# Optimization experiments

Hardware: AMD Instinct MI355X
Metric: run time of the kernel (lower is better)

## Reference

```python
import jax, jax.numpy as jnp
import numpy as np

B, N, C, H = 8, 1025, 512, 8
G = 32  # grid size; S = G*G = N-1


def setup_inputs() -> dict:
    key = jax.random.key(0)
    ks = jax.random.split(key, 5)
    return {
        "x": jax.random.normal(ks[0], (B, N, C), dtype=jnp.float32),
        "qkv_w": jax.random.normal(ks[1], (3 * C, C), dtype=jnp.float32) * (C ** -0.5),
        "proj_w": jax.random.normal(ks[2], (C, C), dtype=jnp.float32) * (C ** -0.5),
        "proj_b": jnp.zeros((C,), dtype=jnp.float32),
        "wg_w": jax.random.normal(ks[3], (H, 64), dtype=jnp.float32) * 0.125,
        "wg_b": jnp.zeros((H,), dtype=jnp.float32),
    }


def _geometry_bias(wg_w, wg_b):
    # BoxRelationalEmbedding on a fixed 32x32 grid; batch-independent, so computed once.
    S = G * G
    xs = jnp.arange(G, dtype=jnp.float32)
    px = jnp.repeat(xs, G)   # px_min: row index per flattened cell
    py = jnp.tile(xs, G)     # py_min: col index per flattened cell
    rx0, ry0 = px / G, py / G
    rx1, ry1 = (px + 1.0) / G, (py + 1.0) / G
    cx = 0.5 * (rx0 + rx1)
    cy = 0.5 * (ry0 + ry1)
    w = rx1 - rx0 + 1.0
    h = ry1 - ry0 + 1.0
    dx = jnp.log(jnp.clip(jnp.abs((cx[:, None] - cx[None, :]) / w[:, None]), 1e-3, None))
    dy = jnp.log(jnp.clip(jnp.abs((cy[:, None] - cy[None, :]) / h[:, None]), 1e-3, None))
    dw = jnp.log(w[:, None] / w[None, :])
    dh = jnp.log(h[:, None] / h[None, :])
    pos = jnp.stack([dx, dy, dw, dh], axis=-1)  # [S,S,4]
    dim_mat = 1.0 / jnp.power(1000.0, jnp.arange(8, dtype=jnp.float32) / 8.0)  # dim_g/8 = 8 freqs
    mul = (100.0 * pos)[..., None] * dim_mat        # [S,S,4,8]
    mul = mul.reshape(S, S, 32)
    emb = jnp.concatenate([jnp.sin(mul), jnp.cos(mul)], axis=-1)  # [S,S,64]
    rgw = jax.nn.relu(jnp.einsum('ijd,hd->hij', emb, wg_w) + wg_b[:, None, None])  # [H,S,S]
    rgw = jnp.log(jnp.clip(rgw, 1e-6, None))
    # pad zero column (dim 3 cat of t1) then zero row (dim 2 cat of t2) -> [H, S+1, S+1]
    return jnp.pad(rgw, ((0, 0), (1, 0), (1, 0)))


def reference(x, qkv_w, proj_w, proj_b, wg_w, wg_b):
    b, n, c = x.shape
    hd = c // H
    scale = hd ** -0.5
    bias = _geometry_bias(wg_w, wg_b)  # [H, n, n]
    qkv = (x @ qkv_w.T).reshape(b, n, 3, H, hd)
    q, k, v = qkv[:, :, 0], qkv[:, :, 1], qkv[:, :, 2]  # each [b,n,H,hd]
    attn = jnp.einsum('bihd,bjhd->bhij', q, k) * scale + bias[None]
    attn = jax.nn.softmax(attn, axis=-1)
    out = jnp.einsum('bhij,bjhd->bihd', attn, v).reshape(b, n, c)
    return out @ proj_w.T + proj_b
```

## Files before the change

kernel.cpp:

```cpp
#include <hip/hip_runtime.h>
#include <hip/hip_bf16.h>
#include <math.h>

#define B_  8
#define N_  1025
#define C_  512
#define H_  8
#define HD_ 64
#define M_  (B_ * N_)
#define VCS 2048
#define VST 36

typedef __attribute__((ext_vector_type(8))) short short8;
typedef __attribute__((ext_vector_type(4))) float f32x4;

__device__ inline unsigned short bf16u(float x) {
    __hip_bfloat16 t = __float2bfloat16(x);
    return *(unsigned short*)&t;
}
__device__ inline void load_lds16(const void* g, void* l) {
    __builtin_amdgcn_global_load_lds(
        (const __attribute__((address_space(1))) unsigned int*)g,
        (__attribute__((address_space(3))) unsigned int*)l, 16, 0, 0);
}

#define PER_ ((size_t)B_ * H_ * N_ * HD_)
#define SZ_QKVW (3 * C_ * C_)
#define SZ_PRJW (C_ * C_)
#define CAST_BLKS ((4198400 + 786432 + 262144) / 4 / 256)

__global__ void prep_kernel(const float* __restrict__ x,
                            const float* __restrict__ qkv_w,
                            const float* __restrict__ proj_w,
                            const float* __restrict__ wg_w,
                            const float* __restrict__ wg_b,
                            unsigned short* __restrict__ xb,
                            unsigned short* __restrict__ wqkvb,
                            unsigned short* __restrict__ wprjb,
                            float* __restrict__ tab) {
    int blk = blockIdx.x;
    int tid = threadIdx.x;
    if (blk < 32) {
        int idx = blk * 256 + tid;
        int h = idx >> 10;
        int a = (idx >> 5) & 31;
        int b = idx & 31;
        float dx = logf(fmaxf((float)a * (1.0f / 33.0f), 0.001f));
        float dy = logf(fmaxf((float)b * (1.0f / 33.0f), 0.001f));
        const float* w = wg_w + h * 64;
        float acc = wg_b[h];
#pragma unroll
        for (int k = 0; k < 8; k++) {
            float f = powf(1000.0f, -(float)k * 0.125f);
            float X = 100.0f * dx * f;
            float Y = 100.0f * dy * f;
            acc += w[k]      * sinf(X);
            acc += w[8 + k]  * sinf(Y);
            acc += w[32 + k] * cosf(X);
            acc += w[40 + k] * cosf(Y);
            acc += w[48 + k] + w[56 + k];
        }
        tab[idx] = logf(fmaxf(fmaxf(acc, 0.0f), 1e-6f));
        return;
    }
    long i4 = ((long)(blk - 32) * 256 + tid) * 4;
    const float* src;
    unsigned short* dst;
    long off;
    if (i4 < (long)PER_)                    { src = x;      dst = xb;    off = i4; }
    else if (i4 < (long)PER_ + SZ_QKVW)     { src = qkv_w;  dst = wqkvb; off = i4 - PER_; }
    else                                    { src = proj_w; dst = wprjb; off = i4 - PER_ - SZ_QKVW; }
    float4 v = *(const float4*)(src + off);
    ushort4 p;
    p.x = bf16u(v.x); p.y = bf16u(v.y); p.z = bf16u(v.z); p.w = bf16u(v.w);
    *(ushort4*)(dst + off) = p;
}

#define GK 512

__global__ __launch_bounds__(256) void gemm_qkv_mfma(
        const unsigned short* __restrict__ A, const unsigned short* __restrict__ W,
        unsigned short* __restrict__ qb, unsigned short* __restrict__ kb,
        unsigned short* __restrict__ vtc) {
    __shared__ __align__(16) unsigned short As[128 * 32];
    __shared__ __align__(16) unsigned short Bs[128 * 32];
    int tid = threadIdx.x;
    int w = tid >> 6, lane = tid & 63;
    int quad = lane >> 4, l16 = lane & 15;
    int m0 = blockIdx.y * 128;
    int n0 = blockIdx.x * 128;
    int wr = (w >> 1) * 64, wc = (w & 1) * 64;

    int c0 = tid, c1 = tid + 256;
    int a_r0 = min(m0 + (c0 >> 2), M_ - 1), a_c0 = (c0 & 3) * 8;
    int a_r1 = min(m0 + (c1 >> 2), M_ - 1), a_c1 = (c1 & 3) * 8;
    int b_r0 = n0 + (c0 >> 2), b_r1 = n0 + (c1 >> 2);

    int which = n0 >> 9;
    int h = ((n0 + wc) >> 6) & 7;

    f32x4 acc[4][4];
    const f32x4 zero4 = {0.f, 0.f, 0.f, 0.f};
#pragma unroll
    for (int mi = 0; mi < 4; mi++)
#pragma unroll
        for (int ni = 0; ni < 4; ni++) acc[mi][ni] = zero4;

    if (which < 2) {
        for (int k0 = 0; k0 < GK; k0 += 32) {
            __syncthreads();
            load_lds16(A + (size_t)a_r0 * GK + k0 + a_c0, &As[w * 512]);
            load_lds16(A + (size_t)a_r1 * GK + k0 + a_c1, &As[2048 + w * 512]);
            load_lds16(W + (size_t)b_r0 * GK + k0 + a_c0, &Bs[w * 512]);
            load_lds16(W + (size_t)b_r1 * GK + k0 + a_c1, &Bs[2048 + w * 512]);
            __syncthreads();
            short8 af[4], bf[4];
#pragma unroll
            for (int mi = 0; mi < 4; mi++)
                af[mi] = *(const short8*)&As[(wr + mi * 16 + l16) * 32 + quad * 8];
#pragma unroll
            for (int ni = 0; ni < 4; ni++)
                bf[ni] = *(const short8*)&Bs[(wc + ni * 16 + l16) * 32 + quad * 8];
#pragma unroll
            for (int mi = 0; mi < 4; mi++)
#pragma unroll
                for (int ni = 0; ni < 4; ni++)
                    acc[mi][ni] = __builtin_amdgcn_mfma_f32_16x16x32_bf16(
                        bf[ni], af[mi], acc[mi][ni], 0, 0, 0);
        }
        unsigned short* dst = (which == 0) ? qb : kb;
        float sc = (which == 0) ? 0.125f : 1.0f;
#pragma unroll
        for (int mi = 0; mi < 4; mi++) {
            int m = m0 + wr + mi * 16 + l16;
            if (m < M_) {
                int bb = m / N_;
                int i  = m - bb * N_;
                unsigned short* row = dst + ((size_t)(bb * H_ + h) * N_ + i) * HD_;
#pragma unroll
                for (int ni = 0; ni < 4; ni++) {
                    ushort4 pk;
                    pk.x = bf16u(acc[mi][ni][0] * sc);
                    pk.y = bf16u(acc[mi][ni][1] * sc);
                    pk.z = bf16u(acc[mi][ni][2] * sc);
                    pk.w = bf16u(acc[mi][ni][3] * sc);
                    *(ushort4*)(row + ni * 16 + quad * 4) = pk;
                }
            }
        }
    } else {
        for (int k0 = 0; k0 < GK; k0 += 32) {
            __syncthreads();
            load_lds16(A + (size_t)a_r0 * GK + k0 + a_c0, &As[w * 512]);
            load_lds16(A + (size_t)a_r1 * GK + k0 + a_c1, &As[2048 + w * 512]);
            load_lds16(W + (size_t)b_r0 * GK + k0 + a_c0, &Bs[w * 512]);
            load_lds16(W + (size_t)b_r1 * GK + k0 + a_c1, &Bs[2048 + w * 512]);
            __syncthreads();
            short8 af[4], bf[4];
#pragma unroll
            for (int mi = 0; mi < 4; mi++)
                af[mi] = *(const short8*)&As[(wr + mi * 16 + l16) * 32 + quad * 8];
#pragma unroll
            for (int ni = 0; ni < 4; ni++)
                bf[ni] = *(const short8*)&Bs[(wc + ni * 16 + l16) * 32 + quad * 8];
#pragma unroll
            for (int mi = 0; mi < 4; mi++)
#pragma unroll
                for (int ni = 0; ni < 4; ni++)
                    acc[mi][ni] = __builtin_amdgcn_mfma_f32_16x16x32_bf16(
                        af[mi], bf[ni], acc[mi][ni], 0, 0, 0);
        }
#pragma unroll
        for (int mi = 0; mi < 4; mi++)
#pragma unroll
            for (int reg = 0; reg < 4; reg++) {
                int m = m0 + wr + mi * 16 + quad * 4 + reg;
                if (m < M_) {
                    int bb = m / N_;
                    int i  = m - bb * N_;
                    int ch = i >> 5, key = i & 31;
                    size_t base = ((size_t)(bb * H_ + h) * VST + ch) * VCS + key;
#pragma unroll
                    for (int ni = 0; ni < 4; ni++)
                        vtc[base + (size_t)(ni * 16 + l16) * 32] = bf16u(acc[mi][ni][reg]);
                }
            }
    }
}

__global__ __launch_bounds__(256) void gemm_proj_mfma(
        const unsigned short* __restrict__ A, const unsigned short* __restrict__ W,
        const float* __restrict__ bias, float* __restrict__ out) {
    __shared__ __align__(16) unsigned short As[128 * 32];
    __shared__ __align__(16) unsigned short Bs[128 * 32];
    int tid = threadIdx.x;
    int w = tid >> 6, lane = tid & 63;
    int quad = lane >> 4, l16 = lane & 15;
    int m0 = blockIdx.y * 128;
    int n0 = blockIdx.x * 128;
    int wr = (w >> 1) * 64, wc = (w & 1) * 64;

    int c0 = tid, c1 = tid + 256;
    int a_r0 = min(m0 + (c0 >> 2), M_ - 1), a_c0 = (c0 & 3) * 8;
    int a_r1 = min(m0 + (c1 >> 2), M_ - 1), a_c1 = (c1 & 3) * 8;
    int b_r0 = n0 + (c0 >> 2), b_r1 = n0 + (c1 >> 2);

    f32x4 acc[4][4];
    const f32x4 zero4 = {0.f, 0.f, 0.f, 0.f};
#pragma unroll
    for (int mi = 0; mi < 4; mi++)
#pragma unroll
        for (int ni = 0; ni < 4; ni++) acc[mi][ni] = zero4;

    for (int k0 = 0; k0 < GK; k0 += 32) {
        __syncthreads();
        load_lds16(A + (size_t)a_r0 * GK + k0 + a_c0, &As[w * 512]);
        load_lds16(A + (size_t)a_r1 * GK + k0 + a_c1, &As[2048 + w * 512]);
        load_lds16(W + (size_t)b_r0 * GK + k0 + a_c0, &Bs[w * 512]);
        load_lds16(W + (size_t)b_r1 * GK + k0 + a_c1, &Bs[2048 + w * 512]);
        __syncthreads();
        short8 af[4], bf[4];
#pragma unroll
        for (int mi = 0; mi < 4; mi++)
            af[mi] = *(const short8*)&As[(wr + mi * 16 + l16) * 32 + quad * 8];
#pragma unroll
        for (int ni = 0; ni < 4; ni++)
            bf[ni] = *(const short8*)&Bs[(wc + ni * 16 + l16) * 32 + quad * 8];
#pragma unroll
        for (int mi = 0; mi < 4; mi++)
#pragma unroll
            for (int ni = 0; ni < 4; ni++)
                acc[mi][ni] = __builtin_amdgcn_mfma_f32_16x16x32_bf16(
                    af[mi], bf[ni], acc[mi][ni], 0, 0, 0);
    }

    float bvals[4];
#pragma unroll
    for (int ni = 0; ni < 4; ni++) bvals[ni] = bias[n0 + wc + ni * 16 + l16];
#pragma unroll
    for (int mi = 0; mi < 4; mi++)
#pragma unroll
        for (int reg = 0; reg < 4; reg++) {
            int m = m0 + wr + mi * 16 + quad * 4 + reg;
            if (m < M_) {
                float* row = out + (size_t)m * C_ + n0 + wc;
#pragma unroll
                for (int ni = 0; ni < 4; ni++)
                    row[ni * 16 + l16] = acc[mi][ni][reg] + bvals[ni];
            }
        }
}

#define RT_ 144

__global__ __launch_bounds__(576) void attn_fused(
        const unsigned short* __restrict__ qg,
        const unsigned short* __restrict__ kg,
        const unsigned short* __restrict__ vtc,
        const float* __restrict__ tab,
        unsigned short* __restrict__ ob) {
    __shared__ __align__(16) unsigned short Ks[2][8192];
    __shared__ __align__(16) unsigned short Vs[2][8192];
    __shared__ __align__(16) unsigned short Pw[9][16 * 40];
    __shared__ float tabs[1089];

    int tid = threadIdx.x;
    int w = tid >> 6, lane = tid & 63;
    int quad = lane >> 4, l16 = lane & 15;

    int lin = blockIdx.x;
    int xcd = lin & 7;
    int u = lin >> 3;
    int bhi = u & 7;
    int mt = u >> 3;
    int bh = xcd * 8 + bhi;
    int b = bh >> 3, h = bh & 7;

    const unsigned short* qp = qg + (size_t)bh * N_ * HD_;
    const unsigned short* kp = kg + (size_t)bh * N_ * HD_;
    const unsigned short* vp = vtc + (size_t)bh * VST * VCS;

    for (int i = tid; i < 1024; i += 576)
        tabs[(i >> 5) * 33 + (i & 31)] = tab[h * 1024 + i];

    short8 qf[2];
    {
        int row = min(mt * RT_ + w * 16 + l16, N_ - 1);
        qf[0] = *(const short8*)(qp + (size_t)row * HD_ + quad * 8);
        qf[1] = *(const short8*)(qp + (size_t)row * HD_ + 32 + quad * 8);
    }

    int rpx[4], rpy[4];
    bool rz[4];
#pragma unroll
    for (int reg = 0; reg < 4; reg++) {
        int r = mt * RT_ + w * 16 + quad * 4 + reg;
        int ri = min(max(r - 1, 0), N_ - 2);
        rpx[reg] = ri >> 5;
        rpy[reg] = ri & 31;
        rz[reg] = (r == 0);
    }

    f32x4 o_acc[4], l_acc;
    const f32x4 zero4 = {0.f, 0.f, 0.f, 0.f};
#pragma unroll
    for (int g2 = 0; g2 < 4; g2++) o_acc[g2] = zero4;
    l_acc = zero4;
    short8 ones;
    {
        short one_bf = (short)0x3F80;
#pragma unroll
        for (int j = 0; j < 8; j++) ones[j] = one_bf;
    }

    auto stage = [&](int t, int buf) {
        if (w < 8) {
#pragma unroll
            for (int r2 = 0; r2 < 2; r2++) {
                int ch = r2 * 512 + tid;
                int ct = ch >> 7, rem = ch & 127;
                int oct = rem >> 4, k16 = rem & 15;
                int key = min(t * 128 + ct * 16 + k16, N_ - 1);
                load_lds16(kp + (size_t)key * HD_ + oct * 8,
                           &Ks[buf][(r2 * 512 + w * 64) * 8]);
                load_lds16(vp + ((size_t)t * 4 * VCS) + (size_t)ch * 8,
                           &Vs[buf][(r2 * 512 + w * 64) * 8]);
            }
        }
    };

    stage(0, 0);

#pragma unroll 1
    for (int t = 0; t < 9; t++) {
        int buf = t & 1;
        __syncthreads();
        if (t < 8) stage(t + 1, buf ^ 1);

        f32x4 s[8];
#pragma unroll
        for (int ct = 0; ct < 8; ct++) {
            short8 b0 = *(const short8*)&Ks[buf][(ct * 128 + quad * 16 + l16) * 8];
            short8 b1 = *(const short8*)&Ks[buf][(ct * 128 + (4 + quad) * 16 + l16) * 8];
            s[ct] = __builtin_amdgcn_mfma_f32_16x16x32_bf16(qf[0], b0, zero4, 0, 0, 0);
            s[ct] = __builtin_amdgcn_mfma_f32_16x16x32_bf16(qf[1], b1, s[ct], 0, 0, 0);
        }

#pragma unroll
        for (int ks = 0; ks < 4; ks++) {
#pragma unroll
            for (int ctl = 0; ctl < 2; ctl++) {
                int ct = ks * 2 + ctl;
                int col = t * 128 + ct * 16 + l16;
                int ji = col - 1;
                int cx = ji >> 5, cy = ji & 31;
                bool cz = (col == 0), co = (col >= N_);
#pragma unroll
                for (int reg = 0; reg < 4; reg++) {
                    float bia = 0.f;
                    if (!rz[reg] && !cz) {
                        int da = __sad(rpx[reg], cx, 0u);
                        int db = __sad(rpy[reg], cy, 0u);
                        bia = tabs[da * 33 + db];
                    }
                    float p = co ? 0.f : __expf(s[ct][reg] + bia);
                    Pw[w][(quad * 4 + reg) * 40 + ctl * 16 + l16] = bf16u(p);
                }
            }
            short8 pf = *(const short8*)&Pw[w][l16 * 40 + quad * 8];
            const unsigned short* vcp = &Vs[buf][ks * 2048 + quad * 8];
#pragma unroll
            for (int g2 = 0; g2 < 4; g2++) {
                short8 vf = *(const short8*)(vcp + (g2 * 16 + l16) * 32);
                o_acc[g2] = __builtin_amdgcn_mfma_f32_16x16x32_bf16(
                    pf, vf, o_acc[g2], 0, 0, 0);
            }
            l_acc = __builtin_amdgcn_mfma_f32_16x16x32_bf16(pf, ones, l_acc, 0, 0, 0);
        }
    }

#pragma unroll
    for (int reg = 0; reg < 4; reg++) {
        int r = mt * RT_ + w * 16 + quad * 4 + reg;
        if (r < N_) {
            float inv = 1.0f / l_acc[reg];
            unsigned short* orow = ob + ((size_t)b * N_ + r) * C_ + h * HD_ + l16;
#pragma unroll
            for (int g2 = 0; g2 < 4; g2++)
                orow[g2 * 16] = bf16u(o_acc[g2][reg] * inv);
        }
    }
}

extern "C" void kernel_launch(void* const* d_in, const int* in_sizes, int n_in,
                              void* d_out, int out_size, void* d_ws, size_t ws_size,
                              hipStream_t stream) {
    const float* x      = (const float*)d_in[0];
    const float* qkv_w  = (const float*)d_in[1];
    const float* proj_w = (const float*)d_in[2];
    const float* proj_b = (const float*)d_in[3];
    const float* wg_w   = (const float*)d_in[4];
    const float* wg_b   = (const float*)d_in[5];
    float* out = (float*)d_out;

    const size_t per = PER_;
    char* ws = (char*)d_ws;
    float* tab            = (float*)ws;
    unsigned short* xb    = (unsigned short*)(ws + (32 << 10));
    unsigned short* wqkvb = xb + per;
    unsigned short* wprjb = wqkvb + (size_t)SZ_QKVW;
    unsigned short* qb    = wprjb + (size_t)SZ_PRJW;
    unsigned short* kb    = qb + per;
    unsigned short* vtc   = kb + per;
    unsigned short* ob    = vtc + (size_t)64 * VST * VCS;

    prep_kernel<<<32 + CAST_BLKS, 256, 0, stream>>>(x, qkv_w, proj_w, wg_w, wg_b,
                                                    xb, wqkvb, wprjb, tab);
    gemm_qkv_mfma<<<dim3(12, 65), 256, 0, stream>>>(xb, wqkvb, qb, kb, vtc);
    attn_fused<<<8 * 8 * 8, 576, 0, stream>>>(qb, kb, vtc, tab, ob);
    gemm_proj_mfma<<<dim3(4, 65), 256, 0, stream>>>(ob, wprjb, proj_b, out);
}
```

Baseline: 210.4 us.

## Swizzle V tile LDS layout and unify QKV GEMM loop with transposed V store

The QKV GEMM now runs a single k-loop with swapped MFMA operands for all three outputs. The V branch writes the transposed chunked layout from the swapped accumulator orientation, so each lane stores consecutive keys instead of strided scalars. In the attention kernel the V tile is loaded into LDS with an XOR swizzle of its 16-byte chunks, and the reads apply the same permutation, to cut LDS bank conflicts when fetching V fragments. The swizzle must match exactly between the global gather and the LDS reads or the output will be wrong.

```diff
diff --git a/kernel.cpp b/kernel.cpp
--- a/kernel.cpp
+++ b/kernel.cpp
@@ -106,28 +106,29 @@
 #pragma unroll
         for (int ni = 0; ni < 4; ni++) acc[mi][ni] = zero4;
 
+    for (int k0 = 0; k0 < GK; k0 += 32) {
+        __syncthreads();
+        load_lds16(A + (size_t)a_r0 * GK + k0 + a_c0, &As[w * 512]);
+        load_lds16(A + (size_t)a_r1 * GK + k0 + a_c1, &As[2048 + w * 512]);
+        load_lds16(W + (size_t)b_r0 * GK + k0 + a_c0, &Bs[w * 512]);
+        load_lds16(W + (size_t)b_r1 * GK + k0 + a_c1, &Bs[2048 + w * 512]);
+        __syncthreads();
+        short8 af[4], bf[4];
+#pragma unroll
+        for (int mi = 0; mi < 4; mi++)
+            af[mi] = *(const short8*)&As[(wr + mi * 16 + l16) * 32 + quad * 8];
+#pragma unroll
+        for (int ni = 0; ni < 4; ni++)
+            bf[ni] = *(const short8*)&Bs[(wc + ni * 16 + l16) * 32 + quad * 8];
+#pragma unroll
+        for (int mi = 0; mi < 4; mi++)
+#pragma unroll
+            for (int ni = 0; ni < 4; ni++)
+                acc[mi][ni] = __builtin_amdgcn_mfma_f32_16x16x32_bf16(
+                    bf[ni], af[mi], acc[mi][ni], 0, 0, 0);
+    }
+
     if (which < 2) {
-        for (int k0 = 0; k0 < GK; k0 += 32) {
-            __syncthreads();
-            load_lds16(A + (size_t)a_r0 * GK + k0 + a_c0, &As[w * 512]);
-            load_lds16(A + (size_t)a_r1 * GK + k0 + a_c1, &As[2048 + w * 512]);
-            load_lds16(W + (size_t)b_r0 * GK + k0 + a_c0, &Bs[w * 512]);
-            load_lds16(W + (size_t)b_r1 * GK + k0 + a_c1, &Bs[2048 + w * 512]);
-            __syncthreads();
-            short8 af[4], bf[4];
-#pragma unroll
-            for (int mi = 0; mi < 4; mi++)
-                af[mi] = *(const short8*)&As[(wr + mi * 16 + l16) * 32 + quad * 8];
-#pragma unroll
-            for (int ni = 0; ni < 4; ni++)
-                bf[ni] = *(const short8*)&Bs[(wc + ni * 16 + l16) * 32 + quad * 8];
-#pragma unroll
-            for (int mi = 0; mi < 4; mi++)
-#pragma unroll
-                for (int ni = 0; ni < 4; ni++)
-                    acc[mi][ni] = __builtin_amdgcn_mfma_f32_16x16x32_bf16(
-                        bf[ni], af[mi], acc[mi][ni], 0, 0, 0);
-        }
         unsigned short* dst = (which == 0) ? qb : kb;
         float sc = (which == 0) ? 0.125f : 1.0f;
 #pragma unroll
@@ -149,42 +150,21 @@
             }
         }
     } else {
-        for (int k0 = 0; k0 < GK; k0 += 32) {
-            __syncthreads();
-            load_lds16(A + (size_t)a_r0 * GK + k0 + a_c0, &As[w * 512]);
-            load_lds16(A + (size_t)a_r1 * GK + k0 + a_c1, &As[2048 + w * 512]);
-            load_lds16(W + (size_t)b_r0 * GK + k0 + a_c0, &Bs[w * 512]);
-            load_lds16(W + (size_t)b_r1 * GK + k0 + a_c1, &Bs[2048 + w * 512]);
-            __syncthreads();
-            short8 af[4], bf[4];
-#pragma unroll
-            for (int mi = 0; mi < 4; mi++)
-                af[mi] = *(const short8*)&As[(wr + mi * 16 + l16) * 32 + quad * 8];
-#pragma unroll
-            for (int ni = 0; ni < 4; ni++)
-                bf[ni] = *(const short8*)&Bs[(wc + ni * 16 + l16) * 32 + quad * 8];
-#pragma unroll
-            for (int mi = 0; mi < 4; mi++)
+#pragma unroll
+        for (int mi = 0; mi < 4; mi++) {
+            int m = m0 + wr + mi * 16 + l16;
+            if (m < M_) {
+                int bb = m / N_;
+                int i  = m - bb * N_;
+                int ch = i >> 5, key = i & 31;
+                unsigned short* base = vtc + ((size_t)(bb * H_ + h) * VST + ch) * VCS + key;
 #pragma unroll
                 for (int ni = 0; ni < 4; ni++)
-                    acc[mi][ni] = __builtin_amdgcn_mfma_f32_16x16x32_bf16(
-                        af[mi], bf[ni], acc[mi][ni], 0, 0, 0);
-        }
-#pragma unroll
-        for (int mi = 0; mi < 4; mi++)
-#pragma unroll
-            for (int reg = 0; reg < 4; reg++) {
-                int m = m0 + wr + mi * 16 + quad * 4 + reg;
-                if (m < M_) {
-                    int bb = m / N_;
-                    int i  = m - bb * N_;
-                    int ch = i >> 5, key = i & 31;
-                    size_t base = ((size_t)(bb * H_ + h) * VST + ch) * VCS + key;
-#pragma unroll
-                    for (int ni = 0; ni < 4; ni++)
-                        vtc[base + (size_t)(ni * 16 + l16) * 32] = bf16u(acc[mi][ni][reg]);
-                }
-            }
+#pragma unroll
+                    for (int reg = 0; reg < 4; reg++)
+                        base[(ni * 16 + quad * 4 + reg) * 32] = bf16u(acc[mi][ni][reg]);
+            }
+        }
     }
 }
 
@@ -317,13 +297,14 @@
         if (w < 8) {
 #pragma unroll
             for (int r2 = 0; r2 < 2; r2++) {
-                int ch = r2 * 512 + tid;
-                int ct = ch >> 7, rem = ch & 127;
+                int s = r2 * 512 + tid;
+                int ct = s >> 7, rem = s & 127;
                 int oct = rem >> 4, k16 = rem & 15;
                 int key = min(t * 128 + ct * 16 + k16, N_ - 1);
                 load_lds16(kp + (size_t)key * HD_ + oct * 8,
                            &Ks[buf][(r2 * 512 + w * 64) * 8]);
-                load_lds16(vp + ((size_t)t * 4 * VCS) + (size_t)ch * 8,
+                int g = s ^ ((s >> 3) & 7);
+                load_lds16(vp + ((size_t)t * 4 * VCS) + (size_t)g * 8,
                            &Vs[buf][(r2 * 512 + w * 64) * 8]);
             }
         }
@@ -368,10 +349,11 @@
                 }
             }
             short8 pf = *(const short8*)&Pw[w][l16 * 40 + quad * 8];
-            const unsigned short* vcp = &Vs[buf][ks * 2048 + quad * 8];
 #pragma unroll
             for (int g2 = 0; g2 < 4; g2++) {
-                short8 vf = *(const short8*)(vcp + (g2 * 16 + l16) * 32);
+                int c = (g2 * 16 + l16) * 4 + quad;
+                int cs = c ^ ((c >> 3) & 7);
+                short8 vf = *(const short8*)&Vs[buf][(ks * 256 + cs) * 8];
                 o_acc[g2] = __builtin_amdgcn_mfma_f32_16x16x32_bf16(
                     pf, vf, o_acc[g2], 0, 0, 0);
             }
```

New measurement: 203.4 us. 3.3% less time.
